# Kernel optimization log

Hardware: AMD Instinct MI355X
Metric: run time of the kernel (lower is better)

## Reference

```python
import jax, jax.numpy as jnp
import numpy as np

EPS = 1e-5
C_M, C, C_Z = 256, 32, 128
N_SEQ, N_RES = 256, 1024


def setup_inputs() -> dict:
    key = jax.random.key(0)
    k1, k2, k3 = jax.random.split(key, 3)
    msa = jax.random.normal(k1, (N_SEQ, N_RES, C_M), dtype=jnp.float32)
    norm_w = jnp.ones((C_M,), dtype=jnp.float32)
    norm_b = jnp.zeros((C_M,), dtype=jnp.float32)
    w_ab = jax.random.normal(k2, (C, C_M), dtype=jnp.float32) * (1.0 / np.sqrt(C_M))
    b_ab = jnp.zeros((C,), dtype=jnp.float32)
    w_out = jax.random.normal(k3, (C_Z, C * C), dtype=jnp.float32) * (1.0 / C)
    b_out = jnp.zeros((C_Z,), dtype=jnp.float32)
    return {"msa": msa, "norm_w": norm_w, "norm_b": norm_b,
            "w_ab": w_ab, "b_ab": b_ab, "w_out": w_out, "b_out": b_out}


def reference(msa, norm_w, norm_b, w_ab, b_ab, w_out, b_out):
    # msa: (s, r, c_m) -> (r, s, c_m)
    x = jnp.transpose(msa, (1, 0, 2))
    s = x.shape[1]
    # LayerNorm over c_m
    mu = jnp.mean(x, axis=-1, keepdims=True)
    var = jnp.mean(jnp.square(x - mu), axis=-1, keepdims=True)
    xn = (x - mu) * jax.lax.rsqrt(var + EPS) * norm_w + norm_b
    # a == b: same linear applied twice to same input in the original
    a = jnp.einsum('rsm,cm->rsc', xn, w_ab) + b_ab          # (r, s, c)
    # mean over s of outer product == batched A^T A / s  -> (r, c, c)
    o = jnp.einsum('rsx,rsy->rxy', a, a) / s
    o = o.reshape(o.shape[0], C * C)                        # (r, c*c)
    pre_pair = jnp.einsum('rk,zk->rz', o, w_out) + b_out    # (r, c_z)
    r = pre_pair.shape[0]
    # unsqueeze(1).expand(r, r, c_z)
    pair = jnp.broadcast_to(pre_pair[:, None, :], (r, r, C_Z))
    return pair
```

## Files before the change

### kernel.cpp

```cpp
#include <hip/hip_runtime.h>

#define NSEQ 256
#define NRES 1024
#define CM   256
#define CC   32
#define CZ   128
#define EPS  1e-5f
#define SROW (NRES * CM)

typedef float f4v __attribute__((ext_vector_type(4)));
typedef __attribute__((ext_vector_type(8))) short short8;
typedef __attribute__((ext_vector_type(4))) float f32x4;
typedef unsigned int u32;

__device__ __forceinline__ float trunc_bf16(float f) {
    return __uint_as_float(__float_as_uint(f) & 0xffff0000u);
}
__device__ __forceinline__ u32 pk_bf16(float a, float b) {
    return (__float_as_uint(b) & 0xffff0000u) | (__float_as_uint(a) >> 16);
}

__global__ void opm_setup(const float* __restrict__ nw,
                          const float* __restrict__ nb,
                          const float* __restrict__ w_ab,
                          const float* __restrict__ b_ab,
                          float* __restrict__ k12,
                          unsigned short* __restrict__ wb_su)
{
    __shared__ float wls[CM * CC];
    const int t = threadIdx.x;
    const float nwm = nw[t];
    #pragma unroll
    for (int c = 0; c < CC; ++c)
        wls[t * CC + c] = nwm * w_ab[c * CM + t];
    __syncthreads();
    if (t < CC) {
        float k1 = 0.f, k2 = 0.f;
        for (int m = 0; m < CM; ++m) {
            k1 += wls[m * CC + t];
            k2 = fmaf(nb[m], w_ab[t * CM + m], k2);
        }
        k12[t]      = k1;
        k12[CC + t] = k2 + b_ab[t];
    }
    for (int e = t; e < 16384; e += 256) {
        const int j     = e & 7;
        const int l     = (e >> 3) & 63;
        const int split = (e >> 9) & 1;
        const int nt    = (e >> 10) & 1;
        const int kk    = e >> 11;
        const int m = (kk << 5) + ((l >> 4) << 3) + j;
        const int c = (nt << 4) + (l & 15);
        const float w  = wls[m * CC + c];
        const float w1 = trunc_bf16(w);
        const float v  = split ? (w - w1) : w;
        wb_su[e] = (unsigned short)(__float_as_uint(v) >> 16);
    }
}

__launch_bounds__(256, 3)
__global__ void opm_compute(const float* __restrict__ msa,
                            const u32*  __restrict__ wb_g,
                            const float* __restrict__ k12,
                            const float* __restrict__ w_out,
                            const float* __restrict__ b_out,
                            float* __restrict__ pre_out)
{
    __shared__ u32 wbl[8192];
    __shared__ float scr[4352];
    __shared__ float st[512];

    const int tid = threadIdx.x;
    const int r   = blockIdx.x;
    const int w   = tid >> 6;
    const int l   = tid & 63;
    const int lr  = l & 15;
    const int lk  = l >> 4;

    const float* xr = msa + (size_t)r * CM;
    size_t rowoff[4];
    #pragma unroll
    for (int mt = 0; mt < 4; ++mt)
        rowoff[mt] = (size_t)((w << 6) + (mt << 4) + lr) * SROW + (lk << 3);

    #pragma unroll
    for (int k = 0; k < 8; ++k) {
        const int i = (tid + (k << 8)) << 2;
        *(f4v*)&wbl[i] = *(const f4v*)&wb_g[i];
    }

    f32x4 acc[4][2];
    #pragma unroll
    for (int mt = 0; mt < 4; ++mt) { acc[mt][0] = (f32x4)0.f; acc[mt][1] = (f32x4)0.f; }
    float psum[4], pssq[4];
    #pragma unroll
    for (int mt = 0; mt < 4; ++mt) { psum[mt] = 0.f; pssq[mt] = 0.f; }

    float4 curA[4], curB[4], nxtA[4], nxtB[4];
    #pragma unroll
    for (int mt = 0; mt < 4; ++mt) {
        curA[mt] = *(const float4*)(xr + rowoff[mt]);
        curB[mt] = *(const float4*)(xr + rowoff[mt] + 4);
    }

    __syncthreads();

    #pragma unroll 1
    for (int kk = 0; kk < 8; ++kk) {
        if (kk < 7) {
            const int o = (kk + 1) << 5;
            #pragma unroll
            for (int mt = 0; mt < 4; ++mt) {
                nxtA[mt] = *(const float4*)(xr + rowoff[mt] + o);
                nxtB[mt] = *(const float4*)(xr + rowoff[mt] + o + 4);
            }
        }
        short8 B[2][2];
        #pragma unroll
        for (int nt = 0; nt < 2; ++nt)
            #pragma unroll
            for (int sp = 0; sp < 2; ++sp) {
                const int fb = ((((kk << 1) + nt) << 1) + sp) * 256 + (l << 2);
                B[nt][sp] = __builtin_bit_cast(short8, *(const f4v*)&wbl[fb]);
            }
        #pragma unroll
        for (int mt = 0; mt < 4; ++mt) {
            const float4 pa = curA[mt], pb = curB[mt];
            psum[mt] += ((pa.x + pa.y) + (pa.z + pa.w)) + ((pb.x + pb.y) + (pb.z + pb.w));
            pssq[mt]  = fmaf(pa.x, pa.x, fmaf(pa.y, pa.y, fmaf(pa.z, pa.z, fmaf(pa.w, pa.w, pssq[mt]))));
            pssq[mt]  = fmaf(pb.x, pb.x, fmaf(pb.y, pb.y, fmaf(pb.z, pb.z, fmaf(pb.w, pb.w, pssq[mt]))));
            uint4 u1, u2;
            u1.x = pk_bf16(pa.x, pa.y); u1.y = pk_bf16(pa.z, pa.w);
            u1.z = pk_bf16(pb.x, pb.y); u1.w = pk_bf16(pb.z, pb.w);
            u2.x = pk_bf16(pa.x - trunc_bf16(pa.x), pa.y - trunc_bf16(pa.y));
            u2.y = pk_bf16(pa.z - trunc_bf16(pa.z), pa.w - trunc_bf16(pa.w));
            u2.z = pk_bf16(pb.x - trunc_bf16(pb.x), pb.y - trunc_bf16(pb.y));
            u2.w = pk_bf16(pb.z - trunc_bf16(pb.z), pb.w - trunc_bf16(pb.w));
            const short8 A1 = __builtin_bit_cast(short8, u1);
            const short8 A2 = __builtin_bit_cast(short8, u2);
            acc[mt][0] = __builtin_amdgcn_mfma_f32_16x16x32_bf16(A1, B[0][0], acc[mt][0], 0, 0, 0);
            acc[mt][1] = __builtin_amdgcn_mfma_f32_16x16x32_bf16(A1, B[1][0], acc[mt][1], 0, 0, 0);
            acc[mt][0] = __builtin_amdgcn_mfma_f32_16x16x32_bf16(A1, B[0][1], acc[mt][0], 0, 0, 0);
            acc[mt][1] = __builtin_amdgcn_mfma_f32_16x16x32_bf16(A1, B[1][1], acc[mt][1], 0, 0, 0);
            acc[mt][0] = __builtin_amdgcn_mfma_f32_16x16x32_bf16(A2, B[0][0], acc[mt][0], 0, 0, 0);
            acc[mt][1] = __builtin_amdgcn_mfma_f32_16x16x32_bf16(A2, B[1][0], acc[mt][1], 0, 0, 0);
        }
        if (kk < 7) {
            #pragma unroll
            for (int mt = 0; mt < 4; ++mt) { curA[mt] = nxtA[mt]; curB[mt] = nxtB[mt]; }
        }
    }

    #pragma unroll
    for (int mt = 0; mt < 4; ++mt) {
        float s1 = psum[mt], s2 = pssq[mt];
        s1 += __shfl_xor(s1, 16); s1 += __shfl_xor(s1, 32);
        s2 += __shfl_xor(s2, 16); s2 += __shfl_xor(s2, 32);
        if (l < 16) {
            const int s = (w << 6) + (mt << 4) + lr;
            const float mu  = s1 * (1.f / CM);
            const float var = s2 * (1.f / CM) - mu * mu;
            st[s]       = mu;
            st[256 + s] = 1.f / sqrtf(var + EPS);
        }
    }
    __syncthreads();

    float* aB = (float*)wbl;
    {
        const int cl = lr;
        const float k1_0 = k12[cl],      k1_1 = k12[16 + cl];
        const float k2_0 = k12[CC + cl], k2_1 = k12[CC + 16 + cl];
        #pragma unroll
        for (int mt = 0; mt < 4; ++mt) {
            #pragma unroll
            for (int rg = 0; rg < 4; ++rg) {
                const int s = (w << 6) + (mt << 4) + (lk << 2) + rg;
                const float mu = st[s], rs = st[256 + s];
                const float a0 = fmaf(rs, acc[mt][0][rg] - mu * k1_0, k2_0);
                const float a1 = fmaf(rs, acc[mt][1][rg] - mu * k1_1, k2_1);
                const int sw = s & 7;
                aB[s * CC + (((cl >> 2) ^ sw) << 2) + (cl & 3)]       = a0;
                aB[s * CC + ((((cl >> 2) + 4) ^ sw) << 2) + (cl & 3)] = a1;
            }
        }
    }
    __syncthreads();

    const int grp = w;
    const int xs_ = (tid >> 3) & 7;
    const int ys_ = tid & 7;
    float4 pr0 = {0,0,0,0}, pr1 = {0,0,0,0}, pr2 = {0,0,0,0}, pr3 = {0,0,0,0};
    #pragma unroll 4
    for (int si = 0; si < 64; ++si) {
        const int s  = (grp << 6) + si;
        const int sw = s & 7;
        const float4 ax = *(const float4*)&aB[s * CC + ((xs_ ^ sw) << 2)];
        const float4 ay = *(const float4*)&aB[s * CC + ((ys_ ^ sw) << 2)];
        pr0.x = fmaf(ax.x, ay.x, pr0.x); pr0.y = fmaf(ax.x, ay.y, pr0.y);
        pr0.z = fmaf(ax.x, ay.z, pr0.z); pr0.w = fmaf(ax.x, ay.w, pr0.w);
        pr1.x = fmaf(ax.y, ay.x, pr1.x); pr1.y = fmaf(ax.y, ay.y, pr1.y);
        pr1.z = fmaf(ax.y, ay.z, pr1.z); pr1.w = fmaf(ax.y, ay.w, pr1.w);
        pr2.x = fmaf(ax.z, ay.x, pr2.x); pr2.y = fmaf(ax.z, ay.y, pr2.y);
        pr2.z = fmaf(ax.z, ay.z, pr2.z); pr2.w = fmaf(ax.z, ay.w, pr2.w);
        pr3.x = fmaf(ax.w, ay.x, pr3.x); pr3.y = fmaf(ax.w, ay.y, pr3.y);
        pr3.z = fmaf(ax.w, ay.z, pr3.z); pr3.w = fmaf(ax.w, ay.w, pr3.w);
    }
    {
        float* pb = &scr[(grp << 10) + ((xs_ << 2) * CC) + (ys_ << 2)];
        *(float4*)&pb[0 * CC] = pr0;
        *(float4*)&pb[1 * CC] = pr1;
        *(float4*)&pb[2 * CC] = pr2;
        *(float4*)&pb[3 * CC] = pr3;
    }
    __syncthreads();
    {
        const float inv_s = 1.f / NSEQ;
        float4 a4 = *(const float4*)&scr[(tid << 2)];
        const float4 b1 = *(const float4*)&scr[1024 + (tid << 2)];
        const float4 b2 = *(const float4*)&scr[2048 + (tid << 2)];
        const float4 b3 = *(const float4*)&scr[3072 + (tid << 2)];
        a4.x = (a4.x + b1.x + b2.x + b3.x) * inv_s;
        a4.y = (a4.y + b1.y + b2.y + b3.y) * inv_s;
        a4.z = (a4.z + b1.z + b2.z + b3.z) * inv_s;
        a4.w = (a4.w + b1.w + b2.w + b3.w) * inv_s;
        *(float4*)&scr[tid << 2] = a4;
    }
    __syncthreads();

    {
        const int z    = tid & 127;
        const int half = tid >> 7;
        const float* wrow = w_out + (size_t)z * (CC * CC) + half * 512;
        const float* op   = &scr[half * 512];
        float po = 0.f;
        #pragma unroll 8
        for (int k = 0; k < 512; k += 4) {
            const float4 o4 = *(const float4*)&op[k];
            const float4 w4 = *(const float4*)&wrow[k];
            po = fmaf(o4.x, w4.x, fmaf(o4.y, w4.y, fmaf(o4.z, w4.z, fmaf(o4.w, w4.w, po))));
        }
        scr[4096 + (half << 7) + z] = po;
    }
    __syncthreads();
    if (tid < CZ)
        pre_out[(size_t)r * CZ + tid] = scr[4096 + tid] + scr[4096 + CZ + tid] + b_out[tid];
}

__launch_bounds__(256, 8)
__global__ void opm_bcast(const float* __restrict__ pre,
                          float* __restrict__ out)
{
    const int bid = blockIdx.x;
    const int r   = bid >> 3;
    const int jb  = bid & 7;
    const int z4  = threadIdx.x & 31;
    const int jo  = threadIdx.x >> 5;

    const f4v pv = *((const f4v*)(pre + (size_t)r * CZ) + z4);
    f4v* outp = (f4v*)out + ((size_t)r * NRES + (size_t)jb * 128) * (CZ / 4);
    for (int j0 = 0; j0 < 128; j0 += 8)
        __builtin_nontemporal_store(pv, &outp[(size_t)(j0 + jo) * (CZ / 4) + z4]);
}

extern "C" void kernel_launch(void* const* d_in, const int* in_sizes, int n_in,
                              void* d_out, int out_size, void* d_ws, size_t ws_size,
                              hipStream_t stream) {
    const float* msa   = (const float*)d_in[0];
    const float* nw    = (const float*)d_in[1];
    const float* nb    = (const float*)d_in[2];
    const float* w_ab  = (const float*)d_in[3];
    const float* b_ab  = (const float*)d_in[4];
    const float* w_out = (const float*)d_in[5];
    const float* b_out = (const float*)d_in[6];
    float* out = (float*)d_out;

    float* pre = (float*)d_ws;
    float* k12 = pre + (size_t)NRES * CZ;
    unsigned short* wb_su = (unsigned short*)(k12 + 64);

    opm_setup<<<1, 256, 0, stream>>>(nw, nb, w_ab, b_ab, k12, wb_su);
    opm_compute<<<NRES, 256, 0, stream>>>(msa, (const u32*)wb_su, k12, w_out, b_out, pre);
    opm_bcast<<<NRES * 8, 256, 0, stream>>>(pre, out);
}
```

Measured before the change: 789.0 us.

## Stage MSA rows through padded LDS with per-thread contiguous loads, B from global

```diff
diff --git a/kernel.cpp b/kernel.cpp
--- a/kernel.cpp
+++ b/kernel.cpp
@@ -7,6 +7,7 @@
 #define CZ   128
 #define EPS  1e-5f
 #define SROW (NRES * CM)
+#define XST  68
 
 typedef float f4v __attribute__((ext_vector_type(4)));
 typedef __attribute__((ext_vector_type(8))) short short8;
@@ -58,7 +59,7 @@
     }
 }
 
-__launch_bounds__(256, 3)
+__launch_bounds__(256, 2)
 __global__ void opm_compute(const float* __restrict__ msa,
                             const u32*  __restrict__ wb_g,
                             const float* __restrict__ k12,
@@ -66,8 +67,7 @@
                             const float* __restrict__ b_out,
                             float* __restrict__ pre_out)
 {
-    __shared__ u32 wbl[8192];
-    __shared__ float scr[4352];
+    __shared__ float xp[NSEQ * XST];
     __shared__ float st[512];
 
     const int tid = threadIdx.x;
@@ -77,96 +77,81 @@
     const int lr  = l & 15;
     const int lk  = l >> 4;
 
-    const float* xr = msa + (size_t)r * CM;
-    size_t rowoff[4];
-    #pragma unroll
-    for (int mt = 0; mt < 4; ++mt)
-        rowoff[mt] = (size_t)((w << 6) + (mt << 4) + lr) * SROW + (lk << 3);
-
-    #pragma unroll
-    for (int k = 0; k < 8; ++k) {
-        const int i = (tid + (k << 8)) << 2;
-        *(f4v*)&wbl[i] = *(const f4v*)&wb_g[i];
-    }
+    const float* xr = msa + (size_t)tid * SROW + (size_t)r * CM;
 
     f32x4 acc[4][2];
     #pragma unroll
     for (int mt = 0; mt < 4; ++mt) { acc[mt][0] = (f32x4)0.f; acc[mt][1] = (f32x4)0.f; }
-    float psum[4], pssq[4];
+    float psum = 0.f, pssq = 0.f;
+
+    float4 nx[16];
     #pragma unroll
-    for (int mt = 0; mt < 4; ++mt) { psum[mt] = 0.f; pssq[mt] = 0.f; }
-
-    float4 curA[4], curB[4], nxtA[4], nxtB[4];
-    #pragma unroll
-    for (int mt = 0; mt < 4; ++mt) {
-        curA[mt] = *(const float4*)(xr + rowoff[mt]);
-        curB[mt] = *(const float4*)(xr + rowoff[mt] + 4);
-    }
-
-    __syncthreads();
+    for (int i = 0; i < 16; ++i)
+        nx[i] = *(const float4*)(xr + (i << 2));
 
     #pragma unroll 1
-    for (int kk = 0; kk < 8; ++kk) {
-        if (kk < 7) {
-            const int o = (kk + 1) << 5;
+    for (int c = 0; c < 4; ++c) {
+        if (c) __syncthreads();
+        #pragma unroll
+        for (int i = 0; i < 16; ++i) {
+            *(float4*)&xp[tid * XST + (i << 2)] = nx[i];
+            psum += (nx[i].x + nx[i].y) + (nx[i].z + nx[i].w);
+            pssq  = fmaf(nx[i].x, nx[i].x, fmaf(nx[i].y, nx[i].y,
+                    fmaf(nx[i].z, nx[i].z, fmaf(nx[i].w, nx[i].w, pssq))));
+        }
+        short8 B[2][2][2];
+        #pragma unroll
+        for (int kk2 = 0; kk2 < 2; ++kk2) {
+            const int kk = (c << 1) + kk2;
+            #pragma unroll
+            for (int nt = 0; nt < 2; ++nt)
+                #pragma unroll
+                for (int sp = 0; sp < 2; ++sp) {
+                    const int fb = ((((kk << 1) + nt) << 1) + sp) * 256 + (l << 2);
+                    B[kk2][nt][sp] = __builtin_bit_cast(short8, *(const f4v*)&wb_g[fb]);
+                }
+        }
+        if (c < 3) {
+            #pragma unroll
+            for (int i = 0; i < 16; ++i)
+                nx[i] = *(const float4*)(xr + ((c + 1) << 6) + (i << 2));
+        }
+        __syncthreads();
+        #pragma unroll
+        for (int kk2 = 0; kk2 < 2; ++kk2) {
             #pragma unroll
             for (int mt = 0; mt < 4; ++mt) {
-                nxtA[mt] = *(const float4*)(xr + rowoff[mt] + o);
-                nxtB[mt] = *(const float4*)(xr + rowoff[mt] + o + 4);
+                const float* ap = &xp[((w << 6) + (mt << 4) + lr) * XST + (kk2 << 5) + (lk << 3)];
+                const float4 pa = *(const float4*)ap;
+                const float4 pb = *(const float4*)(ap + 4);
+                uint4 u1, u2;
+                u1.x = pk_bf16(pa.x, pa.y); u1.y = pk_bf16(pa.z, pa.w);
+                u1.z = pk_bf16(pb.x, pb.y); u1.w = pk_bf16(pb.z, pb.w);
+                u2.x = pk_bf16(pa.x - trunc_bf16(pa.x), pa.y - trunc_bf16(pa.y));
+                u2.y = pk_bf16(pa.z - trunc_bf16(pa.z), pa.w - trunc_bf16(pa.w));
+                u2.z = pk_bf16(pb.x - trunc_bf16(pb.x), pb.y - trunc_bf16(pb.y));
+                u2.w = pk_bf16(pb.z - trunc_bf16(pb.z), pb.w - trunc_bf16(pb.w));
+                const short8 A1 = __builtin_bit_cast(short8, u1);
+                const short8 A2 = __builtin_bit_cast(short8, u2);
+                acc[mt][0] = __builtin_amdgcn_mfma_f32_16x16x32_bf16(A1, B[kk2][0][0], acc[mt][0], 0, 0, 0);
+                acc[mt][1] = __builtin_amdgcn_mfma_f32_16x16x32_bf16(A1, B[kk2][1][0], acc[mt][1], 0, 0, 0);
+                acc[mt][0] = __builtin_amdgcn_mfma_f32_16x16x32_bf16(A1, B[kk2][0][1], acc[mt][0], 0, 0, 0);
+                acc[mt][1] = __builtin_amdgcn_mfma_f32_16x16x32_bf16(A1, B[kk2][1][1], acc[mt][1], 0, 0, 0);
+                acc[mt][0] = __builtin_amdgcn_mfma_f32_16x16x32_bf16(A2, B[kk2][0][0], acc[mt][0], 0, 0, 0);
+                acc[mt][1] = __builtin_amdgcn_mfma_f32_16x16x32_bf16(A2, B[kk2][1][0], acc[mt][1], 0, 0, 0);
             }
         }
-        short8 B[2][2];
-        #pragma unroll
-        for (int nt = 0; nt < 2; ++nt)
-            #pragma unroll
-            for (int sp = 0; sp < 2; ++sp) {
-                const int fb = ((((kk << 1) + nt) << 1) + sp) * 256 + (l << 2);
-                B[nt][sp] = __builtin_bit_cast(short8, *(const f4v*)&wbl[fb]);
-            }
-        #pragma unroll
-        for (int mt = 0; mt < 4; ++mt) {
-            const float4 pa = curA[mt], pb = curB[mt];
-            psum[mt] += ((pa.x + pa.y) + (pa.z + pa.w)) + ((pb.x + pb.y) + (pb.z + pb.w));
-            pssq[mt]  = fmaf(pa.x, pa.x, fmaf(pa.y, pa.y, fmaf(pa.z, pa.z, fmaf(pa.w, pa.w, pssq[mt]))));
-            pssq[mt]  = fmaf(pb.x, pb.x, fmaf(pb.y, pb.y, fmaf(pb.z, pb.z, fmaf(pb.w, pb.w, pssq[mt]))));
-            uint4 u1, u2;
-            u1.x = pk_bf16(pa.x, pa.y); u1.y = pk_bf16(pa.z, pa.w);
-            u1.z = pk_bf16(pb.x, pb.y); u1.w = pk_bf16(pb.z, pb.w);
-            u2.x = pk_bf16(pa.x - trunc_bf16(pa.x), pa.y - trunc_bf16(pa.y));
-            u2.y = pk_bf16(pa.z - trunc_bf16(pa.z), pa.w - trunc_bf16(pa.w));
-            u2.z = pk_bf16(pb.x - trunc_bf16(pb.x), pb.y - trunc_bf16(pb.y));
-            u2.w = pk_bf16(pb.z - trunc_bf16(pb.z), pb.w - trunc_bf16(pb.w));
-            const short8 A1 = __builtin_bit_cast(short8, u1);
-            const short8 A2 = __builtin_bit_cast(short8, u2);
-            acc[mt][0] = __builtin_amdgcn_mfma_f32_16x16x32_bf16(A1, B[0][0], acc[mt][0], 0, 0, 0);
-            acc[mt][1] = __builtin_amdgcn_mfma_f32_16x16x32_bf16(A1, B[1][0], acc[mt][1], 0, 0, 0);
-            acc[mt][0] = __builtin_amdgcn_mfma_f32_16x16x32_bf16(A1, B[0][1], acc[mt][0], 0, 0, 0);
-            acc[mt][1] = __builtin_amdgcn_mfma_f32_16x16x32_bf16(A1, B[1][1], acc[mt][1], 0, 0, 0);
-            acc[mt][0] = __builtin_amdgcn_mfma_f32_16x16x32_bf16(A2, B[0][0], acc[mt][0], 0, 0, 0);
-            acc[mt][1] = __builtin_amdgcn_mfma_f32_16x16x32_bf16(A2, B[1][0], acc[mt][1], 0, 0, 0);
-        }
-        if (kk < 7) {
-            #pragma unroll
-            for (int mt = 0; mt < 4; ++mt) { curA[mt] = nxtA[mt]; curB[mt] = nxtB[mt]; }
-        }
-    }
-
-    #pragma unroll
-    for (int mt = 0; mt < 4; ++mt) {
-        float s1 = psum[mt], s2 = pssq[mt];
-        s1 += __shfl_xor(s1, 16); s1 += __shfl_xor(s1, 32);
-        s2 += __shfl_xor(s2, 16); s2 += __shfl_xor(s2, 32);
-        if (l < 16) {
-            const int s = (w << 6) + (mt << 4) + lr;
-            const float mu  = s1 * (1.f / CM);
-            const float var = s2 * (1.f / CM) - mu * mu;
-            st[s]       = mu;
-            st[256 + s] = 1.f / sqrtf(var + EPS);
-        }
-    }
-    __syncthreads();
-
-    float* aB = (float*)wbl;
+    }
+
+    {
+        const float mu  = psum * (1.f / CM);
+        const float var = pssq * (1.f / CM) - mu * mu;
+        st[tid]       = mu;
+        st[256 + tid] = 1.f / sqrtf(var + EPS);
+    }
+    __syncthreads();
+
+    float* aB = xp;
     {
         const int cl = lr;
         const float k1_0 = k12[cl],      k1_1 = k12[16 + cl];
@@ -187,6 +172,7 @@
     }
     __syncthreads();
 
+    float* scr = xp + 8192;
     const int grp = w;
     const int xs_ = (tid >> 3) & 7;
     const int ys_ = tid & 7;
```

Measured after the change: 791.4 us. Within noise of the previous version (+0.3%).
